# Kernel tuning notes

Measured on AMD Instinct MI355X. Metric: run time of the kernel, lower is better.

Reference implementation:

```python
import jax, jax.numpy as jnp
import numpy as np

K = 9        # kernel_size (neighbors)
GROUPS = 4   # BasicConv uses nn.Conv2d(..., groups=4)


def setup_inputs() -> dict:
    key = jax.random.key(0)
    k1, k2 = jax.random.split(key, 2)
    x = jax.random.normal(k1, (8, 192, 56, 56), dtype=jnp.float32)
    # grouped 1x1 conv: weight (out_channels, 2*in_channels/groups) = (384, 96)
    fan_in = 2 * 192 // GROUPS
    W = jax.random.normal(k2, (384, fan_in), dtype=jnp.float32) * (2.0 / fan_in) ** 0.5
    b = jnp.zeros((384,), dtype=jnp.float32)
    return {"x": x, "W": W, "b": b}


def _knn_idx(xf, k):
    # xf: (B, C, N). L2-normalize channels (F.normalize dim=1), squared euclid dist.
    xn = xf / jnp.maximum(jnp.linalg.norm(xf, axis=1, keepdims=True), 1e-12)
    pts = jnp.transpose(xn, (0, 2, 1))                  # (B, N, C)
    sq = jnp.sum(pts * pts, axis=-1)                    # (B, N)
    dist = sq[:, :, None] - 2.0 * jnp.einsum('bnc,bmc->bnm', pts, pts) + sq[:, None, :]
    _, nn_idx = jax.lax.top_k(-dist, k)                 # (B, N, k) smallest distances
    return nn_idx


def reference(x, W, b):
    B, C, H, Wd = x.shape
    N = H * Wd
    xf = x.reshape(B, C, N)                             # flatten spatial -> graph nodes
    nn_idx = _knn_idx(jax.lax.stop_gradient(xf), K)     # knn built under no_grad in torch
    # gather neighbor features: x_j[b,c,n,k] = xf[b,c,nn_idx[b,n,k]]
    x_j = jax.vmap(lambda f, idx: f[:, idx])(xf, nn_idx)   # (B, C, N, K)
    x_i = jnp.broadcast_to(xf[:, :, :, None], x_j.shape)   # center features
    feat = jnp.concatenate([x_i, x_j - x_i], axis=1)       # (B, 2C, N, K)
    # grouped 1x1 conv (groups=4) + bias + relu
    Cin, Cout = feat.shape[1], W.shape[0]
    fg = feat.reshape(B, GROUPS, Cin // GROUPS, N, K)
    Wg = W.reshape(GROUPS, Cout // GROUPS, Cin // GROUPS)
    out = jnp.einsum('bgcnk,goc->bgonk', fg, Wg).reshape(B, Cout, N, K)
    out = jax.nn.relu(out + b[None, :, None, None])
    out = jnp.max(out, axis=-1)                         # max-aggregate over neighbors
    return out.reshape(B, Cout, H, Wd)
```

## Files before the change

### kernel.cpp

```cpp
#include <hip/hip_runtime.h>
#include <hip/hip_bf16.h>
#include <cstdint>

#define B_ 8
#define C_ 192
#define N_ 3136
#define K_ 9
#define OC_ 384
#define QT_ 49
#define MS_ 4
#define NT_ 49
#define QSZ 24576

typedef unsigned int u32;
typedef _Float16 f16x8 __attribute__((ext_vector_type(8)));
typedef __fp16 h2 __attribute__((ext_vector_type(2)));
typedef float f32x4 __attribute__((ext_vector_type(4)));

#define GLD(g, s) __builtin_amdgcn_global_load_lds( \
    (const __attribute__((address_space(1))) void*)(g), \
    (__attribute__((address_space(3))) void*)(s), 16, 0, 0)

#define WAITV2 asm volatile("s_waitcnt vmcnt(2)" ::: "memory")
#define WAITV0 asm volatile("s_waitcnt vmcnt(0)" ::: "memory")

#define INS(LV, LI, dd, mm) { \
    float cv = (dd); int ci = (mm); \
    _Pragma("unroll") \
    for (int r_ = 0; r_ < 9; ++r_) { \
        bool sw_ = cv < LV[r_]; \
        float tv_ = LV[r_]; int ti_ = LI[r_]; \
        LV[r_] = sw_ ? cv : tv_;  LI[r_] = sw_ ? ci : ti_; \
        cv = sw_ ? tv_ : cv;      ci = sw_ ? ti_ : ci; \
    } }

__global__ __launch_bounds__(64) void prep_k(const float* __restrict__ x,
                                             _Float16* __restrict__ pHL,
                                             float* __restrict__ xT,
                                             float* __restrict__ sq) {
    int g = blockIdx.x * 64 + threadIdx.x;
    int b = g / N_, n = g % N_;
    const float* xb = x + (size_t)b * C_ * N_ + n;
    float ss = 0.f;
    for (int c = 0; c < C_; ++c) { float v = xb[(size_t)c * N_]; ss = fmaf(v, v, ss); }
    float den = fmaxf(sqrtf(ss), 1e-12f);
    float* xrow = xT + (size_t)g * C_;
    _Float16* hrow = pHL + (size_t)g * 384;
    float s2 = 0.f;
    for (int c4 = 0; c4 < 48; ++c4) {
        float4 vv; float* pv = &vv.x;
        union { _Float16 f[4]; uint2 u; } uh, ul;
        #pragma unroll
        for (int j = 0; j < 4; ++j) {
            int c = 4 * c4 + j;
            float v = xb[(size_t)c * N_];
            float p = v / den;
            pv[j] = v;
            _Float16 h = (_Float16)p;
            uh.f[j] = h;
            ul.f[j] = (_Float16)(p - (float)h);
            s2 = fmaf(p, p, s2);
        }
        *(float4*)&xrow[4 * c4] = vv;
        *(uint2*)&hrow[4 * c4] = uh.u;
        *(uint2*)&hrow[192 + 4 * c4] = ul.u;
    }
    sq[g] = s2;
}

__global__ __launch_bounds__(256, 2) void knn_k(const _Float16* __restrict__ pHL,
                                                const float* __restrict__ sq,
                                                float* __restrict__ pkv,
                                                int* __restrict__ pki) {
    __shared__ _Float16 sh[32768];
    float* dist = (float*)(sh + QSZ);
    const int tid = threadIdx.x;
    const int w = tid >> 6, l = tid & 63;
    const int lr = l & 15, lg = l >> 4;
    const int bid = blockIdx.x;
    const int b = bid & 7;
    const int r2_ = bid >> 3;
    const int qt = r2_ >> 2, s4 = r2_ & 3;
    const int q0 = qt * 64;
    const char* hbB = (const char*)(pHL + (size_t)b * N_ * 384);
    const float* sqb = sq + b * N_;

    const int nl = l >> 3, sl = l & 7, ol = sl ^ nl;
    const size_t lane_src = (size_t)nl * 768 + (size_t)(ol >> 2) * 384 + (size_t)(ol & 3) * 16;
    const int slot_h = (lg ^ (lr & 7)) * 8;
    const int slot_l = ((4 | lg) ^ (lr & 7)) * 8;

    float sqq[4][4];
    #pragma unroll
    for (int qs = 0; qs < 4; ++qs)
        #pragma unroll
        for (int r = 0; r < 4; ++r) sqq[qs][r] = sqb[q0 + 16 * qs + 4 * lg + r];

    float lvA[9], lvB[9]; int liA[9], liB[9];
    #pragma unroll
    for (int r = 0; r < 9; ++r) {
        lvA[r] = INFINITY; liA[r] = 0x7fffffff;
        lvB[r] = INFINITY; liB[r] = 0x7fffffff;
    }

    auto stageM = [&](int mt_, int kc_, int buf) {
        size_t mb = (size_t)(mt_ * 64 + w * 16) * 768 + (size_t)kc_ * 64;
        _Float16* md = sh + QSZ + buf * 4096 + w * 1024;
        GLD(hbB + mb + lane_src, md);
        GLD(hbB + mb + 6144 + lane_src, md + 512);
    };

    #pragma unroll
    for (int kc = 0; kc < 6; ++kc) {
        size_t qb = (size_t)(q0 + w * 16) * 768 + (size_t)kc * 64;
        _Float16* qd = sh + kc * 4096 + w * 1024;
        GLD(hbB + qb + lane_src, qd);
        GLD(hbB + qb + 6144 + lane_src, qd + 512);
    }
    __syncthreads();

    for (int mt = s4; mt < NT_; mt += MS_) {
        const int m0 = mt * 64;
        stageM(mt, 0, 0);
        f32x4 acc[4];
        #pragma unroll
        for (int qs = 0; qs < 4; ++qs) acc[qs] = (f32x4)0.f;

        #pragma unroll
        for (int kc = 0; kc < 6; ++kc) {
            if (kc < 5) {
                stageM(mt, kc + 1, (kc + 1) & 1);
                WAITV2;
            } else {
                WAITV0;
            }
            const _Float16* Qb = sh + kc * 4096;
            const _Float16* mrow = sh + QSZ + (kc & 1) * 4096 + (16 * w + lr) * 64;
            f16x8 bh = *(const f16x8*)(mrow + slot_h);
            f16x8 bl = *(const f16x8*)(mrow + slot_l);
            #pragma unroll
            for (int qs = 0; qs < 4; ++qs) {
                const _Float16* qrow = Qb + (16 * qs + lr) * 64;
                f16x8 ah = *(const f16x8*)(qrow + slot_h);
                f16x8 al = *(const f16x8*)(qrow + slot_l);
                acc[qs] = __builtin_amdgcn_mfma_f32_16x16x32_f16(al, bh, acc[qs], 0, 0, 0);
                acc[qs] = __builtin_amdgcn_mfma_f32_16x16x32_f16(ah, bl, acc[qs], 0, 0, 0);
                acc[qs] = __builtin_amdgcn_mfma_f32_16x16x32_f16(ah, bh, acc[qs], 0, 0, 0);
            }
        }
        __syncthreads();

        const float sqm = sqb[m0 + 16 * w + lr];
        {
            const int col = 16 * w + lr;
            #pragma unroll
            for (int qs = 0; qs < 4; ++qs) {
                int gsw = ((4 * qs + lg) ^ lr) << 2;
                float4 v;
                v.x = (sqq[qs][0] - 2.0f * acc[qs][0]) + sqm;
                v.y = (sqq[qs][1] - 2.0f * acc[qs][1]) + sqm;
                v.z = (sqq[qs][2] - 2.0f * acc[qs][2]) + sqm;
                v.w = (sqq[qs][3] - 2.0f * acc[qs][3]) + sqm;
                *(float4*)&dist[col * 64 + gsw] = v;
            }
        }
        __syncthreads();
        const int gq = l >> 2, qe = l & 3;
        #pragma unroll
        for (int jj = 0; jj < 16; ++jj) {
            int col = 16 * w + jj;
            int m = m0 + col;
            float d = dist[col * 64 + ((gq ^ (col & 15)) << 2) + qe];
            if (jj & 1) { INS(lvB, liB, d, m) }
            else        { INS(lvA, liA, d, m) }
        }
        __syncthreads();
    }
    float* Lv = (float*)sh;
    int*   Li = (int*)sh + 4608;
    #pragma unroll
    for (int r = 0; r < 9; ++r) {
        Lv[(tid * 2 + 0) * 9 + r] = lvA[r]; Li[(tid * 2 + 0) * 9 + r] = liA[r];
        Lv[(tid * 2 + 1) * 9 + r] = lvB[r]; Li[(tid * 2 + 1) * 9 + r] = liB[r];
    }
    __syncthreads();
    if (tid < 64) {
        size_t base = ((size_t)((b * QT_ + qt) * MS_ + s4) * 64 + tid) * 9;
        for (int r = 0; r < K_; ++r) {
            float best = INFINITY; int bidx = 0x7fffffff; int bp = 0;
            for (int s = 0; s < 8; ++s) {
                int lb = (((s >> 1) * 64 + tid) * 2 + (s & 1)) * 9;
                for (int e = 0; e < 9; ++e) {
                    float v = Lv[lb + e]; int id = Li[lb + e];
                    if (v < best || (v == best && id < bidx)) { best = v; bidx = id; bp = lb + e; }
                }
            }
            pkv[base + r] = best;
            pki[base + r] = bidx;
            Lv[bp] = INFINITY;
        }
    }
}

__global__ __launch_bounds__(64) void merge_k(const float* __restrict__ pkv,
                                              const int* __restrict__ pki,
                                              int* __restrict__ nn) {
    int g = blockIdx.x * 64 + threadIdx.x;
    int b = g / N_, n = g % N_;
    int qt = n >> 6, q = n & 63;
    float v[MS_ * 9]; int id[MS_ * 9];
    #pragma unroll
    for (int s = 0; s < MS_; ++s) {
        size_t base = ((size_t)((b * QT_ + qt) * MS_ + s) * 64 + q) * 9;
        #pragma unroll
        for (int e = 0; e < 9; ++e) { v[s * 9 + e] = pkv[base + e]; id[s * 9 + e] = pki[base + e]; }
    }
    int* onn = nn + (size_t)g * K_;
    for (int r = 0; r < K_; ++r) {
        float best = INFINITY; int bidx = 0x7fffffff; int bp = 0;
        #pragma unroll
        for (int e = 0; e < MS_ * 9; ++e) {
            if (v[e] < best || (v[e] == best && id[e] < bidx)) { best = v[e]; bidx = id[e]; bp = e; }
        }
        onn[r] = bidx;
        v[bp] = INFINITY;
    }
}

__global__ __launch_bounds__(256) void convi_k(const float* __restrict__ x,
                                               const float* __restrict__ W,
                                               const float* __restrict__ bias,
                                               float* __restrict__ out) {
    __shared__ float Ws[24 * 96];
    const int orange = blockIdx.x & 7;
    const int nb = blockIdx.x >> 3;
    const int tid = threadIdx.x;
    const int g = nb * 256 + tid;
    const int b = g / N_, n = g % N_;
    const int o0 = orange * 24;
    const int cb = (o0 >= 96) ? 96 : 0;
    for (int i = 0; i < 9; ++i) {
        int e = tid + i * 256;
        Ws[e] = W[o0 * 96 + e];
    }
    __syncthreads();
    const float* xb = x + ((size_t)b * C_ + cb) * N_ + n;
    float xi[96];
    #pragma unroll
    for (int c = 0; c < 96; ++c) xi[c] = xb[(size_t)c * N_];
    float* ob = out + ((size_t)b * OC_ + o0) * N_ + n;
    for (int o = 0; o < 24; ++o) {
        float a = bias[o0 + o];
        #pragma unroll
        for (int c4 = 0; c4 < 24; ++c4) {
            float4 w4 = *(const float4*)&Ws[o * 96 + 4 * c4];
            a = fmaf(w4.x, xi[4*c4+0], a);
            a = fmaf(w4.y, xi[4*c4+1], a);
            a = fmaf(w4.z, xi[4*c4+2], a);
            a = fmaf(w4.w, xi[4*c4+3], a);
        }
        ob[(size_t)o * N_] = fmaxf(a, 0.f);
    }
}

__global__ __launch_bounds__(256) void convd_k(const float* __restrict__ xT,
                                               const int* __restrict__ nn,
                                               const float* __restrict__ W,
                                               const float* __restrict__ bias,
                                               float* __restrict__ out) {
    __shared__ _Float16 Wb[192 * 106];
    __shared__ _Float16 dif[4][9 * 192];
    const int tid = threadIdx.x;
    const int w = tid >> 6, l = tid & 63;
    const int b = blockIdx.x / 196;
    const int n0 = (blockIdx.x % 196) * 16;
    const bool hi2 = (l >= 32);

    for (int i = 0; i < 72; ++i) {
        int e = tid + i * 256;
        int row = e / 96, j = e % 96;
        Wb[row * 106 + j] = (_Float16)W[(192 + row) * 96 + j];
    }
    float bo[3];
    #pragma unroll
    for (int oi = 0; oi < 3; ++oi) bo[oi] = bias[192 + l + 64 * oi];
    __syncthreads();

    _Float16* df = dif[w];
    const float* xTb = xT + (size_t)b * N_ * C_;
    float mx0[4], mx1[4], mx2[4];

    #pragma unroll
    for (int r = 0; r < 4; ++r) {
        const int n = n0 + 4 * w + r;
        const float* xin = xTb + (size_t)n * C_;
        float xi0 = xin[l], xi1 = xin[l + 64], xi2 = xin[l + 128];
        const int* nb2 = nn + ((size_t)b * N_ + n) * K_;
        __syncthreads();
        #pragma unroll
        for (int k = 0; k < K_; ++k) {
            int idx = nb2[k];
            const float* xj = xTb + (size_t)idx * C_;
            df[k * 192 + l]       = (_Float16)(xj[l]       - xi0);
            df[k * 192 + l + 64]  = (_Float16)(xj[l + 64]  - xi1);
            df[k * 192 + l + 128] = (_Float16)(xj[l + 128] - xi2);
        }
        __syncthreads();
        float a0[9], a1[9], a2[9];
        #pragma unroll
        for (int k = 0; k < 9; ++k) { a0[k] = 0.f; a1[k] = 0.f; a2[k] = 0.f; }

        for (int jj = 0; jj < 12; ++jj) {
            union U { uint4 u; h2 p[4]; };
            U w0u, w1u, w2u;
            w0u.u = *(const uint4*)(Wb + (size_t)l * 106 + jj * 8);
            w1u.u = *(const uint4*)(Wb + (size_t)(l + 64) * 106 + jj * 8);
            w2u.u = *(const uint4*)(Wb + (size_t)(l + 128) * 106 + jj * 8);
            #pragma unroll
            for (int k = 0; k < 9; ++k) {
                const _Float16* dk = df + k * 192 + jj * 8;
                U dA, dB, dC;
                dA.u = *(const uint4*)(dk);
                dB.u = *(const uint4*)(dk + 96);
                dC.u.x = hi2 ? dB.u.x : dA.u.x;
                dC.u.y = hi2 ? dB.u.y : dA.u.y;
                dC.u.z = hi2 ? dB.u.z : dA.u.z;
                dC.u.w = hi2 ? dB.u.w : dA.u.w;
                #pragma unroll
                for (int p = 0; p < 4; ++p) {
                    a0[k] = __builtin_amdgcn_fdot2(w0u.p[p], dA.p[p], a0[k], false);
                    a1[k] = __builtin_amdgcn_fdot2(w1u.p[p], dC.p[p], a1[k], false);
                    a2[k] = __builtin_amdgcn_fdot2(w2u.p[p], dB.p[p], a2[k], false);
                }
            }
        }
        float m0 = a0[0] + bo[0], m1 = a1[0] + bo[1], m2 = a2[0] + bo[2];
        #pragma unroll
        for (int k = 1; k < 9; ++k) {
            m0 = fmaxf(m0, a0[k] + bo[0]);
            m1 = fmaxf(m1, a1[k] + bo[1]);
            m2 = fmaxf(m2, a2[k] + bo[2]);
        }
        mx0[r] = fmaxf(m0, 0.f); mx1[r] = fmaxf(m1, 0.f); mx2[r] = fmaxf(m2, 0.f);
    }
    float* ob = out + ((size_t)b * OC_ + 192) * N_ + n0 + 4 * w;
    *(float4*)&ob[(size_t)(l)       * N_] = make_float4(mx0[0], mx0[1], mx0[2], mx0[3]);
    *(float4*)&ob[(size_t)(l + 64)  * N_] = make_float4(mx1[0], mx1[1], mx1[2], mx1[3]);
    *(float4*)&ob[(size_t)(l + 128) * N_] = make_float4(mx2[0], mx2[1], mx2[2], mx2[3]);
}

extern "C" void kernel_launch(void* const* d_in, const int* in_sizes, int n_in,
                              void* d_out, int out_size, void* d_ws, size_t ws_size,
                              hipStream_t stream) {
    (void)in_sizes; (void)n_in; (void)out_size; (void)ws_size;
    const float* x    = (const float*)d_in[0];
    const float* W    = (const float*)d_in[1];
    const float* bias = (const float*)d_in[2];
    float* out = (float*)d_out;

    _Float16* pHL = (_Float16*)d_ws;
    float* xT   = (float*)(pHL + (size_t)B_ * N_ * 384);
    float* sq   = xT + (size_t)B_ * N_ * C_;
    int*   nn   = (int*)(sq + (size_t)B_ * N_);
    float* pkv  = (float*)(nn + (size_t)B_ * N_ * K_);
    int*   pki  = (int*)(pkv + (size_t)B_ * QT_ * MS_ * 64 * 9);

    hipLaunchKernelGGL(prep_k,  dim3(392),  dim3(64),  0, stream, x, pHL, xT, sq);
    hipLaunchKernelGGL(knn_k,   dim3(B_ * QT_ * MS_), dim3(256), 0, stream, pHL, sq, pkv, pki);
    hipLaunchKernelGGL(merge_k, dim3(392),  dim3(64),  0, stream, pkv, pki, nn);
    hipLaunchKernelGGL(convi_k, dim3(784),  dim3(256), 0, stream, x, W, bias, out);
    hipLaunchKernelGGL(convd_k, dim3(1568), dim3(256), 0, stream, xT, nn, W, bias, out);
}
```

Before: 673.9 us.

## Halve knn query tile to 32 rows to raise occupancy

Shrinks the per-block query tile in the kNN kernel from 64 to 32 points, which doubles the grid and cuts LDS use from 64KB to 48KB, with launch bounds raised to four blocks per CU. Each thread now keeps a single top-9 list instead of two. The dist buffer layout, swizzle, partial-result indexing and merge kernel are updated to match. The aim is more resident waves and fewer registers per thread, to hide latency in the distance GEMM and the insertion sort. The cost is that every candidate M tile is loaded and processed twice as often per query, so global/LDS traffic for the M side doubles.

```diff
diff --git a/kernel.cpp b/kernel.cpp
--- a/kernel.cpp
+++ b/kernel.cpp
@@ -7,10 +7,10 @@
 #define N_ 3136
 #define K_ 9
 #define OC_ 384
-#define QT_ 49
+#define QT_ 98
 #define MS_ 4
 #define NT_ 49
-#define QSZ 24576
+#define QSZ 12288
 
 typedef unsigned int u32;
 typedef _Float16 f16x8 __attribute__((ext_vector_type(8)));
@@ -68,12 +68,12 @@
     sq[g] = s2;
 }
 
-__global__ __launch_bounds__(256, 2) void knn_k(const _Float16* __restrict__ pHL,
+__global__ __launch_bounds__(256, 4) void knn_k(const _Float16* __restrict__ pHL,
                                                 const float* __restrict__ sq,
                                                 float* __restrict__ pkv,
                                                 int* __restrict__ pki) {
-    __shared__ _Float16 sh[32768];
-    float* dist = (float*)(sh + QSZ);
+    __shared__ _Float16 sh[24576];
+    float* dist = (float*)(sh + 20480);
     const int tid = threadIdx.x;
     const int w = tid >> 6, l = tid & 63;
     const int lr = l & 15, lg = l >> 4;
@@ -81,7 +81,7 @@
     const int b = bid & 7;
     const int r2_ = bid >> 3;
     const int qt = r2_ >> 2, s4 = r2_ & 3;
-    const int q0 = qt * 64;
+    const int q0 = qt * 32;
     const char* hbB = (const char*)(pHL + (size_t)b * N_ * 384);
     const float* sqb = sq + b * N_;
 
@@ -90,18 +90,15 @@
     const int slot_h = (lg ^ (lr & 7)) * 8;
     const int slot_l = ((4 | lg) ^ (lr & 7)) * 8;
 
-    float sqq[4][4];
-    #pragma unroll
-    for (int qs = 0; qs < 4; ++qs)
+    float sqq[2][4];
+    #pragma unroll
+    for (int qs = 0; qs < 2; ++qs)
         #pragma unroll
         for (int r = 0; r < 4; ++r) sqq[qs][r] = sqb[q0 + 16 * qs + 4 * lg + r];
 
-    float lvA[9], lvB[9]; int liA[9], liB[9];
-    #pragma unroll
-    for (int r = 0; r < 9; ++r) {
-        lvA[r] = INFINITY; liA[r] = 0x7fffffff;
-        lvB[r] = INFINITY; liB[r] = 0x7fffffff;
-    }
+    float lv[9]; int li[9];
+    #pragma unroll
+    for (int r = 0; r < 9; ++r) { lv[r] = INFINITY; li[r] = 0x7fffffff; }
 
     auto stageM = [&](int mt_, int kc_, int buf) {
         size_t mb = (size_t)(mt_ * 64 + w * 16) * 768 + (size_t)kc_ * 64;
@@ -112,19 +109,16 @@
 
     #pragma unroll
     for (int kc = 0; kc < 6; ++kc) {
-        size_t qb = (size_t)(q0 + w * 16) * 768 + (size_t)kc * 64;
-        _Float16* qd = sh + kc * 4096 + w * 1024;
-        GLD(hbB + qb + lane_src, qd);
-        GLD(hbB + qb + 6144 + lane_src, qd + 512);
+        size_t qb = (size_t)(q0 + 8 * w) * 768 + (size_t)kc * 64;
+        GLD(hbB + qb + lane_src, sh + kc * 2048 + w * 512);
     }
     __syncthreads();
 
     for (int mt = s4; mt < NT_; mt += MS_) {
         const int m0 = mt * 64;
         stageM(mt, 0, 0);
-        f32x4 acc[4];
-        #pragma unroll
-        for (int qs = 0; qs < 4; ++qs) acc[qs] = (f32x4)0.f;
+        f32x4 acc[2];
+        acc[0] = (f32x4)0.f; acc[1] = (f32x4)0.f;
 
         #pragma unroll
         for (int kc = 0; kc < 6; ++kc) {
@@ -134,12 +128,12 @@
             } else {
                 WAITV0;
             }
-            const _Float16* Qb = sh + kc * 4096;
+            const _Float16* Qb = sh + kc * 2048;
             const _Float16* mrow = sh + QSZ + (kc & 1) * 4096 + (16 * w + lr) * 64;
             f16x8 bh = *(const f16x8*)(mrow + slot_h);
             f16x8 bl = *(const f16x8*)(mrow + slot_l);
             #pragma unroll
-            for (int qs = 0; qs < 4; ++qs) {
+            for (int qs = 0; qs < 2; ++qs) {
                 const _Float16* qrow = Qb + (16 * qs + lr) * 64;
                 f16x8 ah = *(const f16x8*)(qrow + slot_h);
                 f16x8 al = *(const f16x8*)(qrow + slot_l);
@@ -154,42 +148,39 @@
         {
             const int col = 16 * w + lr;
             #pragma unroll
-            for (int qs = 0; qs < 4; ++qs) {
-                int gsw = ((4 * qs + lg) ^ lr) << 2;
+            for (int qs = 0; qs < 2; ++qs) {
+                int g2 = 4 * qs + lg;
+                int gsw = (g2 ^ (col & 7)) << 2;
                 float4 v;
                 v.x = (sqq[qs][0] - 2.0f * acc[qs][0]) + sqm;
                 v.y = (sqq[qs][1] - 2.0f * acc[qs][1]) + sqm;
                 v.z = (sqq[qs][2] - 2.0f * acc[qs][2]) + sqm;
                 v.w = (sqq[qs][3] - 2.0f * acc[qs][3]) + sqm;
-                *(float4*)&dist[col * 64 + gsw] = v;
-            }
-        }
-        __syncthreads();
-        const int gq = l >> 2, qe = l & 3;
-        #pragma unroll
-        for (int jj = 0; jj < 16; ++jj) {
-            int col = 16 * w + jj;
+                *(float4*)&dist[col * 32 + gsw] = v;
+            }
+        }
+        __syncthreads();
+        const int q = tid & 31, seg = tid >> 5;
+        #pragma unroll
+        for (int jj = 0; jj < 8; ++jj) {
+            int col = seg * 8 + jj;
             int m = m0 + col;
-            float d = dist[col * 64 + ((gq ^ (col & 15)) << 2) + qe];
-            if (jj & 1) { INS(lvB, liB, d, m) }
-            else        { INS(lvA, liA, d, m) }
+            float d = dist[col * 32 + (((q >> 2) ^ (col & 7)) << 2) + (q & 3)];
+            INS(lv, li, d, m)
         }
         __syncthreads();
     }
     float* Lv = (float*)sh;
-    int*   Li = (int*)sh + 4608;
-    #pragma unroll
-    for (int r = 0; r < 9; ++r) {
-        Lv[(tid * 2 + 0) * 9 + r] = lvA[r]; Li[(tid * 2 + 0) * 9 + r] = liA[r];
-        Lv[(tid * 2 + 1) * 9 + r] = lvB[r]; Li[(tid * 2 + 1) * 9 + r] = liB[r];
-    }
+    int*   Li = (int*)sh + 2304;
+    #pragma unroll
+    for (int r = 0; r < 9; ++r) { Lv[tid * 9 + r] = lv[r]; Li[tid * 9 + r] = li[r]; }
     __syncthreads();
-    if (tid < 64) {
-        size_t base = ((size_t)((b * QT_ + qt) * MS_ + s4) * 64 + tid) * 9;
+    if (tid < 32) {
+        size_t base = ((size_t)((b * QT_ + qt) * MS_ + s4) * 32 + tid) * 9;
         for (int r = 0; r < K_; ++r) {
             float best = INFINITY; int bidx = 0x7fffffff; int bp = 0;
             for (int s = 0; s < 8; ++s) {
-                int lb = (((s >> 1) * 64 + tid) * 2 + (s & 1)) * 9;
+                int lb = (s * 32 + tid) * 9;
                 for (int e = 0; e < 9; ++e) {
                     float v = Lv[lb + e]; int id = Li[lb + e];
                     if (v < best || (v == best && id < bidx)) { best = v; bidx = id; bp = lb + e; }
@@ -207,11 +198,11 @@
                                               int* __restrict__ nn) {
     int g = blockIdx.x * 64 + threadIdx.x;
     int b = g / N_, n = g % N_;
-    int qt = n >> 6, q = n & 63;
+    int qt = n >> 5, q = n & 31;
     float v[MS_ * 9]; int id[MS_ * 9];
     #pragma unroll
     for (int s = 0; s < MS_; ++s) {
-        size_t base = ((size_t)((b * QT_ + qt) * MS_ + s) * 64 + q) * 9;
+        size_t base = ((size_t)((b * QT_ + qt) * MS_ + s) * 32 + q) * 9;
         #pragma unroll
         for (int e = 0; e < 9; ++e) { v[s * 9 + e] = pkv[base + e]; id[s * 9 + e] = pki[base + e]; }
     }
@@ -363,7 +354,7 @@
     float* sq   = xT + (size_t)B_ * N_ * C_;
     int*   nn   = (int*)(sq + (size_t)B_ * N_);
     float* pkv  = (float*)(nn + (size_t)B_ * N_ * K_);
-    int*   pki  = (int*)(pkv + (size_t)B_ * QT_ * MS_ * 64 * 9);
+    int*   pki  = (int*)(pkv + (size_t)B_ * QT_ * MS_ * 32 * 9);
 
     hipLaunchKernelGGL(prep_k,  dim3(392),  dim3(64),  0, stream, x, pHL, xT, sq);
     hipLaunchKernelGGL(knn_k,   dim3(B_ * QT_ * MS_), dim3(256), 0, stream, pHL, sq, pkv, pki);
```

New measurement: 688.2 us. 2.1% more time.
